# Kernel tuning notes

Measured on AMD Instinct MI355X. Metric: run time of the kernel, lower is better.

Reference implementation:

```python
import jax, jax.numpy as jnp
import numpy as np

B, T, D, H, L = 128, 128, 128, 1024, 3


def gru_cell(x, h, W_ih, W_hh, b_ih, b_hh):
    # PyTorch GRUCell math
    gi = x @ W_ih.T + b_ih            # [B, 3H]
    gh = h @ W_hh.T + b_hh            # [B, 3H]
    i_r, i_z, i_n = jnp.split(gi, 3, axis=-1)
    h_r, h_z, h_n = jnp.split(gh, 3, axis=-1)
    r = jax.nn.sigmoid(i_r + h_r)
    z = jax.nn.sigmoid(i_z + h_z)
    n = jnp.tanh(i_n + r * h_n)
    return (1.0 - z) * n + z * h


def setup_inputs() -> dict:
    key = jax.random.key(0)
    ks = jax.random.split(key, 12)
    k = 1.0 / np.sqrt(H)
    u = lambda kk, shape: jax.random.uniform(kk, shape, jnp.float32, -k, k)
    x = jax.random.normal(ks[0], (B, T, D), jnp.float32)
    masks = jax.random.bernoulli(ks[1], 0.7, (B, T)).astype(jnp.float32)
    return dict(
        x=x, masks=masks,
        W_ih0=u(ks[2], (3 * H, D)), W_hh0=u(ks[3], (3 * H, H)),
        b_ih0=u(ks[4], (3 * H,)), b_hh0=u(ks[5], (3 * H,)),
        W_ih_rest=u(ks[6], (L - 1, 3 * H, H)), W_hh_rest=u(ks[7], (L - 1, 3 * H, H)),
        b_ih_rest=u(ks[8], (L - 1, 3 * H)), b_hh_rest=u(ks[9], (L - 1, 3 * H)),
        Wp=u(ks[10], (D, H)), bp=u(ks[11], (D,)),
    )


def reference(x, masks, W_ih0, W_hh0, b_ih0, b_hh0,
              W_ih_rest, W_hh_rest, b_ih_rest, b_hh_rest, Wp, bp):
    xT = jnp.transpose(x, (1, 0, 2))   # [T, B, D]
    mT = masks.T                       # [T, B]

    def step(carry, inputs):
        h, prev = carry                # prev = completed input at previous step (x[:,0] at t=0)
        x_t, m_t = inputs
        h = gru_cell(prev, h, W_ih0, W_hh0, b_ih0, b_hh0)
        for l in range(L - 1):         # faithful: upper layers use h as both input and hidden
            h = gru_cell(h, h, W_ih_rest[l], W_hh_rest[l], b_ih_rest[l], b_hh_rest[l])
        imp = h @ Wp.T + bp            # [B, D]
        comp = m_t[:, None] * x_t + (1.0 - m_t[:, None]) * imp
        return (h, comp), (imp, comp)

    h0 = jnp.zeros((x.shape[0], H), x.dtype)
    (h_final, _), (imps, comps) = jax.lax.scan(step, (h0, xT[0]), (xT, mT))
    # original only records steps t < T-1
    imputed = jnp.transpose(imps[:-1], (1, 0, 2))    # [B, T-1, D]
    completed = jnp.transpose(comps[:-1], (1, 0, 2))  # [B, T-1, D]
    return h_final, completed, imputed
```

## Files before the change

### kernel.cpp

```cpp
#include <hip/hip_runtime.h>
#include <hip/hip_bf16.h>


typedef __hip_bfloat16 bf16;
typedef unsigned int u32;
typedef unsigned short u16;
typedef __attribute__((ext_vector_type(8))) short v8bf;
typedef __attribute__((ext_vector_type(4))) float v4f;
typedef __attribute__((ext_vector_type(4))) u32 v4u;

__device__ __forceinline__ float bf2f(bf16 v){ return __bfloat162float(v); }
__device__ __forceinline__ bf16 f2bf(float v){ return __float2bfloat16(v); }
__device__ __forceinline__ float sigm(float x){ return 1.f/(1.f + __expf(-x)); }
__device__ __forceinline__ float tanh_(float x){
  float a = fminf(fmaxf(x, -15.f), 15.f);
  float t = __expf(2.f*a);
  return (t-1.f)/(t+1.f);
}
__device__ __forceinline__ v8bf ldv(const bf16* p){ return *reinterpret_cast<const v8bf*>(p); }

__global__ void pack_upper_k(const float* __restrict__ Wih, const float* __restrict__ Whh,
                             bf16* __restrict__ dst){
  int tid = blockIdx.x*256 + threadIdx.x;
  int lane = tid & 63;
  int u    = tid >> 6;
  int kk   = u & 31;
  int j    = (u >> 5) & 63;
  int s    = (u >> 11) & 3;
  int l    = u >> 13;
  int n    = j*16 + (lane & 15);
  int k    = kk*32 + ((lane>>4)&3)*8;
  int row  = (s==0) ? n : (s==1 ? 1024+n : 2048+n);
  size_t src = ((size_t)l*3072 + row)*1024 + k;
  size_t o = (size_t)tid*8;
  #pragma unroll
  for (int e=0;e<8;e++){
    float v;
    if (s < 2)      v = Wih[src+e] + Whh[src+e];
    else if (s==2)  v = Wih[src+e];
    else            v = Whh[src+e];
    dst[o+e] = f2bf(v);
  }
}
__global__ void pack_l0h_k(const float* __restrict__ Whh0, bf16* __restrict__ dst){
  int tid = blockIdx.x*256 + threadIdx.x;
  int lane = tid & 63;
  int u  = tid >> 6;
  int kk = u & 31;
  int j  = (u >> 5) & 63;
  int g  = u >> 11;
  int row = g*1024 + j*16 + (lane&15);
  int k   = kk*32 + ((lane>>4)&3)*8;
  size_t src = (size_t)row*1024 + k;
  size_t o = (size_t)tid*8;
  #pragma unroll
  for (int e=0;e<8;e++) dst[o+e] = f2bf(Whh0[src+e]);
}
__global__ void pack_l0x_k(const float* __restrict__ Wih0, bf16* __restrict__ dst){
  int tid = blockIdx.x*256 + threadIdx.x;
  int lane = tid & 63;
  int u  = tid >> 6;
  int kk = u & 3;
  int j  = (u >> 2) & 63;
  int g  = u >> 8;
  int row = g*1024 + j*16 + (lane&15);
  int k   = kk*32 + ((lane>>4)&3)*8;
  size_t src = (size_t)row*128 + k;
  size_t o = (size_t)tid*8;
  #pragma unroll
  for (int e=0;e<8;e++) dst[o+e] = f2bf(Wih0[src+e]);
}
__global__ void pack_imp_k(const float* __restrict__ Wp, bf16* __restrict__ dst){
  int tid = blockIdx.x*256 + threadIdx.x;
  int lane = tid & 63;
  int u  = tid >> 6;
  int kk = u & 31;
  int jj = u >> 5;
  int row = jj*16 + (lane&15);
  int k   = kk*32 + ((lane>>4)&3)*8;
  size_t src = (size_t)row*1024 + k;
  size_t o = (size_t)tid*8;
  #pragma unroll
  for (int e=0;e<8;e++) dst[o+e] = f2bf(Wp[src+e]);
}
__global__ void init_pk(bf16* __restrict__ hA){
  int tid = blockIdx.x*256 + threadIdx.x;
  hA[tid] = f2bf(0.f);
}

__device__ __forceinline__ v8bf afrag(const bf16* lds_h, int kk, int lane){
  return ldv(lds_h + (size_t)kk*512 + (size_t)lane*8);
}
__device__ __forceinline__ float hp16(const bf16* lds_h, int rl, int colh){
  int kk = colh >> 5, q = (colh >> 3) & 3, e = colh & 7;
  return bf2f(lds_h[(size_t)kk*512 + (size_t)(q*16 + rl)*8 + e]);
}

#define MFMA(a,b,c) __builtin_amdgcn_mfma_f32_16x16x32_bf16((a),(b),(c),0,0,0)

#define T_W(w, row, col)  lds2[(w)*272 + (row)*17 + (col)]

__device__ __forceinline__ void stage16_8(const bf16* __restrict__ src_rg, bf16* lds_h,
                                          int wave, int lane, int l15, int quad){
  const bf16* g0 = src_rg + (size_t)l15*1024 + wave*128 + quad*8;
  v4u r0 = *(const v4u*)(g0);
  v4u r1 = *(const v4u*)(g0 + 32);
  v4u r2 = *(const v4u*)(g0 + 64);
  v4u r3 = *(const v4u*)(g0 + 96);
  bf16* d = lds_h + (size_t)(wave*4)*512 + (size_t)lane*8;
  *(v4u*)(d)        = r0;
  *(v4u*)(d + 512)  = r1;
  *(v4u*)(d + 1024) = r2;
  *(v4u*)(d + 1536) = r3;
}

__global__ __launch_bounds__(512) void gru_l0(
  const int t,
  const float* __restrict__ x, const float* __restrict__ masks,
  const float* __restrict__ bih0, const float* __restrict__ bhh0,
  const float* __restrict__ bp,
  const bf16* __restrict__ packL0h, const bf16* __restrict__ packL0x,
  const bf16* __restrict__ packImp,
  const bf16* __restrict__ hA, bf16* __restrict__ hB,
  float* __restrict__ out)
{
  const int tid  = threadIdx.x;
  const int lane = tid & 63;
  const int wave = tid >> 6;
  const int l15  = lane & 15;
  const int quad = lane >> 4;
  const int bid  = blockIdx.x;
  const int cseg = bid & 31;
  const int g    = bid >> 5;
  const int rB   = g * 16;

  __shared__ bf16 lds_h[16384];
  __shared__ bf16 lds_c[2048];
  __shared__ float lds2[12*272];

  stage16_8(hA + (size_t)rB*1024, lds_h, wave, lane, l15, quad);
  __syncthreads();

  if (t == 0){
    const int rl = tid >> 5, cb = tid & 31;
    #pragma unroll
    for (int k=0;k<4;++k){
      const int d = cb*4 + k;
      float v = x[(size_t)(rB+rl)*16384 + d];
      lds_c[(size_t)(d>>5)*512 + (size_t)(((d>>3)&3)*16 + rl)*8 + (d&7)] = f2bf(v);
    }
  } else {
    {
      const int jt = wave;
      v4f a0 = {0.f,0.f,0.f,0.f}, a1 = {0.f,0.f,0.f,0.f};
      const bf16* wp = packImp + ((size_t)(jt*32))*512 + lane*8;
      #pragma unroll
      for (int i=0;i<32;i+=2){
        a0 = MFMA(afrag(lds_h, i,   lane), ldv(wp + (size_t)i*512),     a0);
        a1 = MFMA(afrag(lds_h, i+1, lane), ldv(wp + (size_t)(i+1)*512), a1);
      }
      const v4f a = a0 + a1;
      #pragma unroll
      for (int r=0;r<4;r++) T_W(jt, quad*4+r, l15) = a[r];
    }
    __syncthreads();
    const int rl = tid >> 5, cb = tid & 31, tm = t - 1;
    const float m = masks[(size_t)(rB+rl)*128 + tm];
    const bool wr = (cb == cseg);
    #pragma unroll
    for (int k=0;k<4;++k){
      const int d = cb*4 + k;
      const int djt = d >> 4, c = d & 15;
      float imp = T_W(djt, rl, c) + bp[d];
      float xv  = x[((size_t)(rB+rl)*128 + tm)*128 + d];
      float cv  = m*xv + (1.f - m)*imp;
      lds_c[(size_t)(d>>5)*512 + (size_t)(((d>>3)&3)*16 + rl)*8 + (d&7)] = f2bf(cv);
      if (wr){
        size_t o = ((size_t)(rB+rl)*127 + tm)*128 + d;
        out[131072 + o]  = cv;
        out[2211840 + o] = imp;
      }
    }
  }
  __syncthreads();

  if (wave < 6){
    const int gg = wave >> 1, jt = wave & 1;
    const int j = cseg*2 + jt;
    v4f a0 = {0.f,0.f,0.f,0.f}, a1 = {0.f,0.f,0.f,0.f};
    const bf16* wp = packL0h + ((size_t)((gg*64 + j)*32))*512 + lane*8;
    #pragma unroll
    for (int i=0;i<32;i+=2){
      a0 = MFMA(afrag(lds_h, i,   lane), ldv(wp + (size_t)i*512),     a0);
      a1 = MFMA(afrag(lds_h, i+1, lane), ldv(wp + (size_t)(i+1)*512), a1);
    }
    const v4f a = a0 + a1;
    #pragma unroll
    for (int r=0;r<4;r++) T_W(wave, quad*4+r, l15) = a[r];
  } else {
    const int jt = wave - 6;
    const int j = cseg*2 + jt;
    #pragma unroll
    for (int gg=0; gg<3; ++gg){
      v4f a = {0.f,0.f,0.f,0.f};
      const bf16* wp = packL0x + ((size_t)((gg*64 + j)*4))*512 + lane*8;
      #pragma unroll
      for (int i=0;i<4;++i){
        a = MFMA(ldv(lds_c + (size_t)i*512 + lane*8), ldv(wp + (size_t)i*512), a);
      }
      const int slot = 6 + gg*2 + jt;
      #pragma unroll
      for (int r=0;r<4;r++) T_W(slot, quad*4+r, l15) = a[r];
    }
  }
  __syncthreads();
  {
    const int rl = tid >> 5, cb = tid & 31;
    const int jt = cb >> 4, c = cb & 15;
    const int col = cseg*32 + cb;
    float ghr = T_W(0*2+jt, rl, c);
    float ghz = T_W(1*2+jt, rl, c);
    float ghn = T_W(2*2+jt, rl, c);
    float gir = T_W(6+0*2+jt, rl, c);
    float giz = T_W(6+1*2+jt, rl, c);
    float gin = T_W(6+2*2+jt, rl, c);
    float rgg = sigm(gir + bih0[col]      + ghr + bhh0[col]);
    float zg  = sigm(giz + bih0[1024+col] + ghz + bhh0[1024+col]);
    float nv  = tanh_(gin + bih0[2048+col] + rgg*(ghn + bhh0[2048+col]));
    float hp  = hp16(lds_h, rl, col);
    hB[(size_t)(rB+rl)*1024 + col] = f2bf((1.f - zg)*nv + zg*hp);
  }
}

__global__ __launch_bounds__(512) void gru_up(
  const int lay, const int t,
  const float* __restrict__ bihR, const float* __restrict__ bhhR,
  const bf16* __restrict__ packU,
  const bf16* __restrict__ src, bf16* __restrict__ dst,
  float* __restrict__ out)
{
  const int tid  = threadIdx.x;
  const int lane = tid & 63;
  const int wave = tid >> 6;
  const int l15  = lane & 15;
  const int quad = lane >> 4;
  const int bid  = blockIdx.x;
  const int cseg = bid & 31;
  const int g    = bid >> 5;
  const int rB   = g * 16;
  const bf16* packL = packU + (size_t)lay*4194304;
  const float* bi = bihR + lay*3072;
  const float* bh = bhhR + lay*3072;
  float* out_h = (lay == 1 && t == 127) ? out : nullptr;

  __shared__ bf16 lds_h[16384];
  __shared__ float lds2[8*272];

  stage16_8(src + (size_t)rB*1024, lds_h, wave, lane, l15, quad);
  __syncthreads();
  {
    const int s = wave >> 1, jt = wave & 1;
    const int j = cseg*2 + jt;
    v4f a0 = {0.f,0.f,0.f,0.f}, a1 = {0.f,0.f,0.f,0.f};
    const bf16* wp = packL + ((size_t)((s*64 + j)*32))*512 + lane*8;
    #pragma unroll
    for (int i=0;i<32;i+=2){
      a0 = MFMA(afrag(lds_h, i,   lane), ldv(wp + (size_t)i*512),     a0);
      a1 = MFMA(afrag(lds_h, i+1, lane), ldv(wp + (size_t)(i+1)*512), a1);
    }
    const v4f a = a0 + a1;
    #pragma unroll
    for (int r=0;r<4;r++) T_W(wave, quad*4+r, l15) = a[r];
  }
  __syncthreads();
  {
    const int rl = tid >> 5, cb = tid & 31;
    const int jt = cb >> 4, c = cb & 15;
    const int col = cseg*32 + cb;
    float pr  = T_W(0*2+jt, rl, c);
    float pz  = T_W(1*2+jt, rl, c);
    float pin = T_W(2*2+jt, rl, c);
    float phn = T_W(3*2+jt, rl, c);
    float rgg = sigm(pr + bi[col] + bh[col]);
    float zg  = sigm(pz + bi[1024+col] + bh[1024+col]);
    float nv  = tanh_(pin + bi[2048+col] + rgg*(phn + bh[2048+col]));
    float hp  = hp16(lds_h, rl, col);
    float hv  = (1.f - zg)*nv + zg*hp;
    dst[(size_t)(rB+rl)*1024 + col] = f2bf(hv);
    if (out_h) out_h[(size_t)(rB+rl)*1024 + col] = hv;
  }
}

extern "C" void kernel_launch(void* const* d_in, const int* in_sizes, int n_in,
                              void* d_out, int out_size, void* d_ws, size_t ws_size,
                              hipStream_t stream)
{
  (void)in_sizes; (void)n_in; (void)out_size; (void)ws_size;
  const float* x     = (const float*)d_in[0];
  const float* masks = (const float*)d_in[1];
  const float* Wih0  = (const float*)d_in[2];
  const float* Whh0  = (const float*)d_in[3];
  const float* bih0  = (const float*)d_in[4];
  const float* bhh0  = (const float*)d_in[5];
  const float* WihR  = (const float*)d_in[6];
  const float* WhhR  = (const float*)d_in[7];
  const float* bihR  = (const float*)d_in[8];
  const float* bhhR  = (const float*)d_in[9];
  const float* Wp    = (const float*)d_in[10];
  const float* bp    = (const float*)d_in[11];
  float* out = (float*)d_out;

  bf16* hA      = (bf16*)((char*)d_ws + 4096);
  bf16* hB      = hA + 131072;
  bf16* hC      = hB + 131072;
  bf16* packU   = hC + 131072;
  bf16* packL0h = packU + 8388608;
  bf16* packL0x = packL0h + 3145728;
  bf16* packImp = packL0x + 393216;

  hipLaunchKernelGGL(init_pk,      dim3(512),  dim3(256), 0, stream, hA);
  hipLaunchKernelGGL(pack_upper_k, dim3(4096), dim3(256), 0, stream, WihR, WhhR, packU);
  hipLaunchKernelGGL(pack_l0h_k,   dim3(1536), dim3(256), 0, stream, Whh0, packL0h);
  hipLaunchKernelGGL(pack_l0x_k,   dim3(192),  dim3(256), 0, stream, Wih0, packL0x);
  hipLaunchKernelGGL(pack_imp_k,   dim3(64),   dim3(256), 0, stream, Wp, packImp);

  for (int t = 0; t < 128; ++t){
    hipLaunchKernelGGL(gru_l0, dim3(256), dim3(512), 0, stream,
        t, x, masks, bih0, bhh0, bp, packL0h, packL0x, packImp, hA, hB, out);
    hipLaunchKernelGGL(gru_up, dim3(256), dim3(512), 0, stream,
        0, t, bihR, bhhR, packU, hB, hC, out);
    hipLaunchKernelGGL(gru_up, dim3(256), dim3(512), 0, stream,
        1, t, bihR, bhhR, packU, hC, hA, out);
  }
}
```

Before: 2.983 ms.

## Retile GRU step kernels to 32 rows by 16 columns per block

```diff
diff --git a/kernel.cpp b/kernel.cpp
--- a/kernel.cpp
+++ b/kernel.cpp
@@ -88,30 +88,33 @@
   hA[tid] = f2bf(0.f);
 }
 
-__device__ __forceinline__ v8bf afrag(const bf16* lds_h, int kk, int lane){
-  return ldv(lds_h + (size_t)kk*512 + (size_t)lane*8);
-}
-__device__ __forceinline__ float hp16(const bf16* lds_h, int rl, int colh){
+__device__ __forceinline__ v8bf afrag32(const bf16* lds_h, int rt, int kk, int lane){
+  return ldv(lds_h + (size_t)rt*16384 + (size_t)kk*512 + (size_t)lane*8);
+}
+__device__ __forceinline__ float hp32(const bf16* lds_h, int rl, int colh){
+  int rt = rl >> 4, lr = rl & 15;
   int kk = colh >> 5, q = (colh >> 3) & 3, e = colh & 7;
-  return bf2f(lds_h[(size_t)kk*512 + (size_t)(q*16 + rl)*8 + e]);
+  return bf2f(lds_h[(size_t)rt*16384 + (size_t)kk*512 + (size_t)(q*16 + lr)*8 + e]);
 }
 
 #define MFMA(a,b,c) __builtin_amdgcn_mfma_f32_16x16x32_bf16((a),(b),(c),0,0,0)
 
 #define T_W(w, row, col)  lds2[(w)*272 + (row)*17 + (col)]
 
-__device__ __forceinline__ void stage16_8(const bf16* __restrict__ src_rg, bf16* lds_h,
-                                          int wave, int lane, int l15, int quad){
-  const bf16* g0 = src_rg + (size_t)l15*1024 + wave*128 + quad*8;
-  v4u r0 = *(const v4u*)(g0);
-  v4u r1 = *(const v4u*)(g0 + 32);
-  v4u r2 = *(const v4u*)(g0 + 64);
-  v4u r3 = *(const v4u*)(g0 + 96);
-  bf16* d = lds_h + (size_t)(wave*4)*512 + (size_t)lane*8;
-  *(v4u*)(d)        = r0;
-  *(v4u*)(d + 512)  = r1;
-  *(v4u*)(d + 1024) = r2;
-  *(v4u*)(d + 1536) = r3;
+__device__ __forceinline__ void stage32(const bf16* __restrict__ src_rg, bf16* lds_h,
+                                        int wave, int lane, int l15, int quad){
+  const int rt = wave >> 2, kq = wave & 3;
+  const bf16* g0 = src_rg + (size_t)(rt*16 + l15)*1024 + kq*256 + quad*8;
+  bf16* d0 = lds_h + (size_t)rt*16384 + (size_t)(kq*8)*512 + (size_t)lane*8;
+  #pragma unroll
+  for (int i=0;i<8;++i){
+    v4u r = *(const v4u*)(g0 + i*32);
+    *(v4u*)(d0 + i*512) = r;
+  }
+}
+
+__device__ __forceinline__ size_t cidx(int rt, int lr, int d){
+  return (size_t)rt*2048 + (size_t)(d>>5)*512 + (size_t)(((d>>3)&3)*16 + lr)*8 + (d&7);
 }
 
 __global__ __launch_bounds__(512) void gru_l0(
@@ -130,52 +133,57 @@
   const int l15  = lane & 15;
   const int quad = lane >> 4;
   const int bid  = blockIdx.x;
-  const int cseg = bid & 31;
-  const int g    = bid >> 5;
-  const int rB   = g * 16;
-
-  __shared__ bf16 lds_h[16384];
-  __shared__ bf16 lds_c[2048];
-  __shared__ float lds2[12*272];
-
-  stage16_8(hA + (size_t)rB*1024, lds_h, wave, lane, l15, quad);
+  const int jj   = bid & 63;
+  const int rg   = bid >> 6;
+  const int rB   = rg * 32;
+
+  __shared__ bf16 lds_h[32768];
+  __shared__ bf16 lds_c[4096];
+  __shared__ float lds2[16*272];
+
+  stage32(hA + (size_t)rB*1024, lds_h, wave, lane, l15, quad);
   __syncthreads();
 
   if (t == 0){
-    const int rl = tid >> 5, cb = tid & 31;
-    #pragma unroll
-    for (int k=0;k<4;++k){
-      const int d = cb*4 + k;
+    const int rl = tid >> 4, c = tid & 15;
+    const int rt = rl >> 4, lr = rl & 15;
+    #pragma unroll
+    for (int k=0;k<8;++k){
+      const int d = c*8 + k;
       float v = x[(size_t)(rB+rl)*16384 + d];
-      lds_c[(size_t)(d>>5)*512 + (size_t)(((d>>3)&3)*16 + rl)*8 + (d&7)] = f2bf(v);
+      lds_c[cidx(rt, lr, d)] = f2bf(v);
     }
   } else {
     {
-      const int jt = wave;
-      v4f a0 = {0.f,0.f,0.f,0.f}, a1 = {0.f,0.f,0.f,0.f};
-      const bf16* wp = packImp + ((size_t)(jt*32))*512 + lane*8;
+      const int rt = wave >> 2, dp = wave & 3;
       #pragma unroll
-      for (int i=0;i<32;i+=2){
-        a0 = MFMA(afrag(lds_h, i,   lane), ldv(wp + (size_t)i*512),     a0);
-        a1 = MFMA(afrag(lds_h, i+1, lane), ldv(wp + (size_t)(i+1)*512), a1);
+      for (int u2=0; u2<2; ++u2){
+        const int jt = dp*2 + u2;
+        v4f a0 = {0.f,0.f,0.f,0.f}, a1 = {0.f,0.f,0.f,0.f};
+        const bf16* wp = packImp + ((size_t)(jt*32))*512 + lane*8;
+        #pragma unroll
+        for (int i=0;i<32;i+=2){
+          a0 = MFMA(afrag32(lds_h, rt, i,   lane), ldv(wp + (size_t)i*512),     a0);
+          a1 = MFMA(afrag32(lds_h, rt, i+1, lane), ldv(wp + (size_t)(i+1)*512), a1);
+        }
+        const v4f a = a0 + a1;
+        #pragma unroll
+        for (int r=0;r<4;r++) T_W(rt*8 + jt, quad*4+r, l15) = a[r];
       }
-      const v4f a = a0 + a1;
-      #pragma unroll
-      for (int r=0;r<4;r++) T_W(jt, quad*4+r, l15) = a[r];
     }
     __syncthreads();
-    const int rl = tid >> 5, cb = tid & 31, tm = t - 1;
+    const int rl = tid >> 4, c = tid & 15, tm = t - 1;
+    const int rt = rl >> 4, lr = rl & 15;
     const float m = masks[(size_t)(rB+rl)*128 + tm];
-    const bool wr = (cb == cseg);
-    #pragma unroll
-    for (int k=0;k<4;++k){
-      const int d = cb*4 + k;
-      const int djt = d >> 4, c = d & 15;
-      float imp = T_W(djt, rl, c) + bp[d];
+    #pragma unroll
+    for (int k=0;k<8;++k){
+      const int d = c*8 + k;
+      const int djt = d >> 4, cc = d & 15;
+      float imp = T_W(rt*8 + djt, lr, cc) + bp[d];
       float xv  = x[((size_t)(rB+rl)*128 + tm)*128 + d];
       float cv  = m*xv + (1.f - m)*imp;
-      lds_c[(size_t)(d>>5)*512 + (size_t)(((d>>3)&3)*16 + rl)*8 + (d&7)] = f2bf(cv);
-      if (wr){
+      lds_c[cidx(rt, lr, d)] = f2bf(cv);
+      if ((d >> 1) == jj){
         size_t o = ((size_t)(rB+rl)*127 + tm)*128 + d;
         out[131072 + o]  = cv;
         out[2211840 + o] = imp;
@@ -185,49 +193,48 @@
   __syncthreads();
 
   if (wave < 6){
-    const int gg = wave >> 1, jt = wave & 1;
-    const int j = cseg*2 + jt;
+    const int gg = wave >> 1, rt = wave & 1;
     v4f a0 = {0.f,0.f,0.f,0.f}, a1 = {0.f,0.f,0.f,0.f};
-    const bf16* wp = packL0h + ((size_t)((gg*64 + j)*32))*512 + lane*8;
+    const bf16* wp = packL0h + ((size_t)((gg*64 + jj)*32))*512 + lane*8;
     #pragma unroll
     for (int i=0;i<32;i+=2){
-      a0 = MFMA(afrag(lds_h, i,   lane), ldv(wp + (size_t)i*512),     a0);
-      a1 = MFMA(afrag(lds_h, i+1, lane), ldv(wp + (size_t)(i+1)*512), a1);
+      a0 = MFMA(afrag32(lds_h, rt, i,   lane), ldv(wp + (size_t)i*512),     a0);
+      a1 = MFMA(afrag32(lds_h, rt, i+1, lane), ldv(wp + (size_t)(i+1)*512), a1);
     }
     const v4f a = a0 + a1;
     #pragma unroll
     for (int r=0;r<4;r++) T_W(wave, quad*4+r, l15) = a[r];
   } else {
-    const int jt = wave - 6;
-    const int j = cseg*2 + jt;
+    const int rt = wave - 6;
     #pragma unroll
     for (int gg=0; gg<3; ++gg){
       v4f a = {0.f,0.f,0.f,0.f};
-      const bf16* wp = packL0x + ((size_t)((gg*64 + j)*4))*512 + lane*8;
+      const bf16* wp = packL0x + ((size_t)((gg*64 + jj)*4))*512 + lane*8;
       #pragma unroll
       for (int i=0;i<4;++i){
-        a = MFMA(ldv(lds_c + (size_t)i*512 + lane*8), ldv(wp + (size_t)i*512), a);
+        a = MFMA(ldv(lds_c + (size_t)rt*2048 + (size_t)i*512 + lane*8),
+                 ldv(wp + (size_t)i*512), a);
       }
-      const int slot = 6 + gg*2 + jt;
+      const int slot = 6 + rt*3 + gg;
       #pragma unroll
       for (int r=0;r<4;r++) T_W(slot, quad*4+r, l15) = a[r];
     }
   }
   __syncthreads();
   {
-    const int rl = tid >> 5, cb = tid & 31;
-    const int jt = cb >> 4, c = cb & 15;
-    const int col = cseg*32 + cb;
-    float ghr = T_W(0*2+jt, rl, c);
-    float ghz = T_W(1*2+jt, rl, c);
-    float ghn = T_W(2*2+jt, rl, c);
-    float gir = T_W(6+0*2+jt, rl, c);
-    float giz = T_W(6+1*2+jt, rl, c);
-    float gin = T_W(6+2*2+jt, rl, c);
+    const int rl = tid >> 4, c = tid & 15;
+    const int rt = rl >> 4, lr = rl & 15;
+    const int col = jj*16 + c;
+    float ghr = T_W(0*2+rt, lr, c);
+    float ghz = T_W(1*2+rt, lr, c);
+    float ghn = T_W(2*2+rt, lr, c);
+    float gir = T_W(6+rt*3+0, lr, c);
+    float giz = T_W(6+rt*3+1, lr, c);
+    float gin = T_W(6+rt*3+2, lr, c);
     float rgg = sigm(gir + bih0[col]      + ghr + bhh0[col]);
     float zg  = sigm(giz + bih0[1024+col] + ghz + bhh0[1024+col]);
     float nv  = tanh_(gin + bih0[2048+col] + rgg*(ghn + bhh0[2048+col]));
-    float hp  = hp16(lds_h, rl, col);
+    float hp  = hp32(lds_h, rl, col);
     hB[(size_t)(rB+rl)*1024 + col] = f2bf((1.f - zg)*nv + zg*hp);
   }
 }
@@ -245,28 +252,27 @@
   const int l15  = lane & 15;
   const int quad = lane >> 4;
   const int bid  = blockIdx.x;
-  const int cseg = bid & 31;
-  const int g    = bid >> 5;
-  const int rB   = g * 16;
+  const int jj   = bid & 63;
+  const int rg   = bid >> 6;
+  const int rB   = rg * 32;
   const bf16* packL = packU + (size_t)lay*4194304;
   const float* bi = bihR + lay*3072;
   const float* bh = bhhR + lay*3072;
   float* out_h = (lay == 1 && t == 127) ? out : nullptr;
 
-  __shared__ bf16 lds_h[16384];
+  __shared__ bf16 lds_h[32768];
   __shared__ float lds2[8*272];
 
-  stage16_8(src + (size_t)rB*1024, lds_h, wave, lane, l15, quad);
+  stage32(src + (size_t)rB*1024, lds_h, wave, lane, l15, quad);
   __syncthreads();
   {
-    const int s = wave >> 1, jt = wave & 1;
-    const int j = cseg*2 + jt;
+    const int rt = wave >> 2, s = wave & 3;
     v4f a0 = {0.f,0.f,0.f,0.f}, a1 = {0.f,0.f,0.f,0.f};
-    const bf16* wp = packL + ((size_t)((s*64 + j)*32))*512 + lane*8;
+    const bf16* wp = packL + ((size_t)((s*64 + jj)*32))*512 + lane*8;
     #pragma unroll
     for (int i=0;i<32;i+=2){
-      a0 = MFMA(afrag(lds_h, i,   lane), ldv(wp + (size_t)i*512),     a0);
-      a1 = MFMA(afrag(lds_h, i+1, lane), ldv(wp + (size_t)(i+1)*512), a1);
+      a0 = MFMA(afrag32(lds_h, rt, i,   lane), ldv(wp + (size_t)i*512),     a0);
+      a1 = MFMA(afrag32(lds_h, rt, i+1, lane), ldv(wp + (size_t)(i+1)*512), a1);
     }
     const v4f a = a0 + a1;
     #pragma unroll
@@ -274,17 +280,17 @@
   }
   __syncthreads();
   {
-    const int rl = tid >> 5, cb = tid & 31;
-    const int jt = cb >> 4, c = cb & 15;
-    const int col = cseg*32 + cb;
-    float pr  = T_W(0*2+jt, rl, c);
-    float pz  = T_W(1*2+jt, rl, c);
-    float pin = T_W(2*2+jt, rl, c);
-    float phn = T_W(3*2+jt, rl, c);
+    const int rl = tid >> 4, c = tid & 15;
+    const int rt = rl >> 4, lr = rl & 15;
+    const int col = jj*16 + c;
+    float pr  = T_W(rt*4+0, lr, c);
+    float pz  = T_W(rt*4+1, lr, c);
+    float pin = T_W(rt*4+2, lr, c);
+    float phn = T_W(rt*4+3, lr, c);
     float rgg = sigm(pr + bi[col] + bh[col]);
     float zg  = sigm(pz + bi[1024+col] + bh[1024+col]);
     float nv  = tanh_(pin + bi[2048+col] + rgg*(phn + bh[2048+col]));
-    float hp  = hp16(lds_h, rl, col);
+    float hp  = hp32(lds_h, rl, col);
     float hv  = (1.f - zg)*nv + zg*hp;
     dst[(size_t)(rB+rl)*1024 + col] = f2bf(hv);
     if (out_h) out_h[(size_t)(rB+rl)*1024 + col] = hv;
```

New measurement: 3.956 ms. 32.6% more time.

## Retile upper GRU layers to 32-row blocks with split-K waves reusing weights

Applied to the files above, without the earlier changes.

```diff
diff --git a/kernel.cpp b/kernel.cpp
--- a/kernel.cpp
+++ b/kernel.cpp
@@ -94,6 +94,14 @@
 __device__ __forceinline__ float hp16(const bf16* lds_h, int rl, int colh){
   int kk = colh >> 5, q = (colh >> 3) & 3, e = colh & 7;
   return bf2f(lds_h[(size_t)kk*512 + (size_t)(q*16 + rl)*8 + e]);
+}
+__device__ __forceinline__ v8bf afrag32(const bf16* lds_h, int rt, int kk, int lane){
+  return ldv(lds_h + (size_t)rt*16384 + (size_t)kk*512 + (size_t)lane*8);
+}
+__device__ __forceinline__ float hp32(const bf16* lds_h, int rl, int colh){
+  int rt = rl >> 4, lr = rl & 15;
+  int kk = colh >> 5, q = (colh >> 3) & 3, e = colh & 7;
+  return bf2f(lds_h[(size_t)rt*16384 + (size_t)kk*512 + (size_t)(q*16 + lr)*8 + e]);
 }
 
 #define MFMA(a,b,c) __builtin_amdgcn_mfma_f32_16x16x32_bf16((a),(b),(c),0,0,0)
@@ -112,6 +120,17 @@
   *(v4u*)(d + 512)  = r1;
   *(v4u*)(d + 1024) = r2;
   *(v4u*)(d + 1536) = r3;
+}
+__device__ __forceinline__ void stage32(const bf16* __restrict__ src_rg, bf16* lds_h,
+                                        int wave, int lane, int l15, int quad){
+  const int rt = wave >> 2, kq = wave & 3;
+  const bf16* g0 = src_rg + (size_t)(rt*16 + l15)*1024 + kq*256 + quad*8;
+  bf16* d0 = lds_h + (size_t)rt*16384 + (size_t)(kq*8)*512 + (size_t)lane*8;
+  #pragma unroll
+  for (int i=0;i<8;++i){
+    v4u r = *(const v4u*)(g0 + i*32);
+    *(v4u*)(d0 + i*512) = r;
+  }
 }
 
 __global__ __launch_bounds__(512) void gru_l0(
@@ -245,46 +264,49 @@
   const int l15  = lane & 15;
   const int quad = lane >> 4;
   const int bid  = blockIdx.x;
-  const int cseg = bid & 31;
-  const int g    = bid >> 5;
-  const int rB   = g * 16;
+  const int jj   = bid & 63;
+  const int rg   = bid >> 6;
+  const int rB   = rg * 32;
   const bf16* packL = packU + (size_t)lay*4194304;
   const float* bi = bihR + lay*3072;
   const float* bh = bhhR + lay*3072;
   float* out_h = (lay == 1 && t == 127) ? out : nullptr;
 
-  __shared__ bf16 lds_h[16384];
-  __shared__ float lds2[8*272];
-
-  stage16_8(src + (size_t)rB*1024, lds_h, wave, lane, l15, quad);
+  __shared__ bf16 lds_h[32768];
+  __shared__ float lds2[16*272];
+
+  stage32(src + (size_t)rB*1024, lds_h, wave, lane, l15, quad);
   __syncthreads();
   {
-    const int s = wave >> 1, jt = wave & 1;
-    const int j = cseg*2 + jt;
+    const int s = wave >> 1, kh = wave & 1;
     v4f a0 = {0.f,0.f,0.f,0.f}, a1 = {0.f,0.f,0.f,0.f};
-    const bf16* wp = packL + ((size_t)((s*64 + j)*32))*512 + lane*8;
-    #pragma unroll
-    for (int i=0;i<32;i+=2){
-      a0 = MFMA(afrag(lds_h, i,   lane), ldv(wp + (size_t)i*512),     a0);
-      a1 = MFMA(afrag(lds_h, i+1, lane), ldv(wp + (size_t)(i+1)*512), a1);
-    }
-    const v4f a = a0 + a1;
-    #pragma unroll
-    for (int r=0;r<4;r++) T_W(wave, quad*4+r, l15) = a[r];
+    const bf16* wp = packL + ((size_t)((s*64 + jj)*32 + kh*16))*512 + lane*8;
+    #pragma unroll
+    for (int i=0;i<16;++i){
+      const int kk = kh*16 + i;
+      v8bf wf = ldv(wp + (size_t)i*512);
+      a0 = MFMA(afrag32(lds_h, 0, kk, lane), wf, a0);
+      a1 = MFMA(afrag32(lds_h, 1, kk, lane), wf, a1);
+    }
+    #pragma unroll
+    for (int r=0;r<4;r++){
+      T_W(kh*8 + s*2 + 0, quad*4+r, l15) = a0[r];
+      T_W(kh*8 + s*2 + 1, quad*4+r, l15) = a1[r];
+    }
   }
   __syncthreads();
   {
-    const int rl = tid >> 5, cb = tid & 31;
-    const int jt = cb >> 4, c = cb & 15;
-    const int col = cseg*32 + cb;
-    float pr  = T_W(0*2+jt, rl, c);
-    float pz  = T_W(1*2+jt, rl, c);
-    float pin = T_W(2*2+jt, rl, c);
-    float phn = T_W(3*2+jt, rl, c);
+    const int rl = tid >> 4, c = tid & 15;
+    const int rt = rl >> 4, lr = rl & 15;
+    const int col = jj*16 + c;
+    float pr  = T_W(0*2+rt, lr, c) + T_W(8+0*2+rt, lr, c);
+    float pz  = T_W(1*2+rt, lr, c) + T_W(8+1*2+rt, lr, c);
+    float pin = T_W(2*2+rt, lr, c) + T_W(8+2*2+rt, lr, c);
+    float phn = T_W(3*2+rt, lr, c) + T_W(8+3*2+rt, lr, c);
     float rgg = sigm(pr + bi[col] + bh[col]);
     float zg  = sigm(pz + bi[1024+col] + bh[1024+col]);
     float nv  = tanh_(pin + bi[2048+col] + rgg*(phn + bh[2048+col]));
-    float hp  = hp16(lds_h, rl, col);
+    float hp  = hp32(lds_h, rl, col);
     float hv  = (1.f - zg)*nv + zg*hp;
     dst[(size_t)(rB+rl)*1024 + col] = f2bf(hv);
     if (out_h) out_h[(size_t)(rB+rl)*1024 + col] = hv;
```

New measurement: 3.149 ms. +5.6%, slower.
